# Optimization experiments

Measured on AMD Instinct MI355X. Metric: run time of the kernel, lower is better.

## Reference

```python
import jax, jax.numpy as jnp
import numpy as np

Q_HEADS, KV_HEADS, HEAD_DIM, WINDOW = 16, 4, 128, 512
HIDDEN = 2048
ROPE_BASE = 10000.0


def _rope_tables(T, head_dim, dtype):
    half = head_dim // 2
    inv_freq = 1.0 / (ROPE_BASE ** (jnp.arange(half, dtype=jnp.float32) / half))
    t = jnp.arange(T, dtype=jnp.float32)
    freqs = jnp.outer(t, inv_freq)  # [T, half]
    return jnp.cos(freqs).astype(dtype), jnp.sin(freqs).astype(dtype)


def _apply_rope(x, cos, sin):
    # x: [B, T, H, D]; cos/sin: [T, D//2] -> broadcast [1, T, 1, D//2]
    c = cos[None, :, None, :]
    s = sin[None, :, None, :]
    x1, x2 = jnp.split(x, 2, axis=-1)
    return jnp.concatenate([x1 * c - x2 * s, x1 * s + x2 * c], axis=-1)


def setup_inputs() -> dict:
    key = jax.random.key(0)
    ks = jax.random.split(key, 5)
    B, T = 1, 4096
    x = jax.random.normal(ks[0], (B, T, HIDDEN), dtype=jnp.float32)
    sc = 0.02
    wq = jax.random.normal(ks[1], (Q_HEADS * HEAD_DIM, HIDDEN), dtype=jnp.float32) * sc
    wk = jax.random.normal(ks[2], (KV_HEADS * HEAD_DIM, HIDDEN), dtype=jnp.float32) * sc
    wv = jax.random.normal(ks[3], (KV_HEADS * HEAD_DIM, HIDDEN), dtype=jnp.float32) * sc
    wo = jax.random.normal(ks[4], (HIDDEN, Q_HEADS * HEAD_DIM), dtype=jnp.float32) * sc
    return {"x": x, "wq": wq, "wk": wk, "wv": wv, "wo": wo}


def reference(x, wq, wk, wv, wo):
    B, T, _ = x.shape
    reps = Q_HEADS // KV_HEADS
    scale = 1.0 / np.sqrt(HEAD_DIM)

    q = jnp.einsum('bth,oh->bto', x, wq).reshape(B, T, Q_HEADS, HEAD_DIM)
    k = jnp.einsum('bth,oh->bto', x, wk).reshape(B, T, KV_HEADS, HEAD_DIM)
    v = jnp.einsum('bth,oh->bto', x, wv).reshape(B, T, KV_HEADS, HEAD_DIM)

    cos, sin = _rope_tables(T, HEAD_DIM, x.dtype)
    q = _apply_rope(q, cos, sin)
    k = _apply_rope(k, cos, sin)

    # GQA without materializing repeated K/V: group q as [B,T,KVH,reps,D]
    qg = q.reshape(B, T, KV_HEADS, reps, HEAD_DIM)
    scores = jnp.einsum('btgrd,bsgd->bgrts', qg, k) * scale  # [B,KVH,reps,T,T]

    idx = jnp.arange(T)
    # allowed: causal (s <= t) AND within window (t - s <= WINDOW)
    allowed = (idx[None, :] <= idx[:, None]) & (idx[:, None] - idx[None, :] <= WINDOW)
    scores = jnp.where(allowed[None, None, None], scores, jnp.finfo(scores.dtype).min)
    probs = jax.nn.softmax(scores, axis=-1)

    out = jnp.einsum('bgrts,bsgd->btgrd', probs, v)  # [B,T,KVH,reps,D]
    out = out.reshape(B, T, Q_HEADS * HEAD_DIM)
    return jnp.einsum('bto,ho->bth', out, wo)
```

## Files before the change

### kernel.cpp

```cpp
#include <hip/hip_runtime.h>

typedef __attribute__((ext_vector_type(8))) short short8;
typedef __attribute__((ext_vector_type(4))) float f32x4;
typedef __attribute__((ext_vector_type(4))) unsigned short u16x4;

__device__ __forceinline__ unsigned short f2b(float f) {
  unsigned int u = __float_as_uint(f);
  u += 0x7fffu + ((u >> 16) & 1u);
  return (unsigned short)(u >> 16);
}
__device__ __forceinline__ void glds16(const void* g, void* l) {
  __builtin_amdgcn_global_load_lds(
      (const __attribute__((address_space(1))) unsigned int*)g,
      (__attribute__((address_space(3))) unsigned int*)l, 16, 0, 0);
}

__global__ __launch_bounds__(256) void cast_all(const float* __restrict__ x,
                                                const float* __restrict__ wq,
                                                const float* __restrict__ wk,
                                                const float* __restrict__ wv,
                                                const float* __restrict__ wo,
                                                unsigned short* __restrict__ dst) {
  const int i = blockIdx.x * 256 + threadIdx.x;
  const float* s;
  int off;
  if (i < 2097152)      { s = x;  off = i; }
  else if (i < 3145728) { s = wq; off = i - 2097152; }
  else if (i < 3407872) { s = wk; off = i - 3145728; }
  else if (i < 3670016) { s = wv; off = i - 3407872; }
  else                  { s = wo; off = i - 3670016; }
  f32x4 v = ((const f32x4*)s)[off];
  u16x4 o;
  o[0] = f2b(v[0]); o[1] = f2b(v[1]); o[2] = f2b(v[2]); o[3] = f2b(v[3]);
  ((u16x4*)dst)[i] = o;
}

__global__ __launch_bounds__(512, 2) void gemm256(
    const unsigned short* __restrict__ A, const unsigned short* __restrict__ B,
    const int K, const int mode,
    unsigned short* __restrict__ qb, unsigned short* __restrict__ kb,
    unsigned short* __restrict__ vtg, float* __restrict__ Cout, const int N) {
  extern __shared__ char smem[];
  const int tid = threadIdx.x;
  const int w = tid >> 6, lane = tid & 63;
  const int quad = lane >> 4, l15 = lane & 15;
  const int wm = w >> 2, wn = w & 3;
  const int m0 = blockIdx.x * 256, n0 = blockIdx.y * 256;
  const int nkt = K >> 6;

  int nb[4];
#pragma unroll
  for (int ni = 0; ni < 4; ++ni) {
    const int bbi = (wn & 1) * 4 + ni;
    nb[ni] = mode ? ((bbi & 1) ? 4 + (bbi >> 1) : (bbi >> 1)) : bbi;
  }

  const int fragOff = l15 * 64 + ((quad * 16) ^ ((l15 & 8) << 2));
  char* const aWave = smem + wm * 16384;
  char* const bWave = smem + 32768 + (wn >> 1) * 16384;

  const int sr = lane >> 2;
  const int sc = ((lane & 3) * 8) ^ ((lane & 32) ? 16 : 0);

  auto stageA = [&](int buf, int h, int kt) {
#pragma unroll
    for (int j = 0; j < 2; ++j) {
      const int s = j * 8 + w;
      glds16(A + (size_t)(m0 + h * 128 + (s >> 1) * 16 + sr) * K + kt * 64 + (s & 1) * 32 + sc,
             smem + buf * 65536 + h * 16384 + s * 1024);
    }
  };
  auto stageB = [&](int buf, int h, int kt) {
#pragma unroll
    for (int j = 0; j < 2; ++j) {
      const int s = j * 8 + w;
      glds16(B + (size_t)(n0 + h * 128 + (s >> 1) * 16 + sr) * K + kt * 64 + (s & 1) * 32 + sc,
             smem + buf * 65536 + 32768 + h * 16384 + s * 1024);
    }
  };

  f32x4 acc[8][4];
  const f32x4 fz = {0.f, 0.f, 0.f, 0.f};
#pragma unroll
  for (int i = 0; i < 8; ++i)
#pragma unroll
    for (int j = 0; j < 4; ++j) acc[i][j] = fz;

  stageB(0, 0, 0); stageA(0, 0, 0); stageA(0, 1, 0); stageB(0, 1, 0);
  stageB(1, 0, 1); stageA(1, 0, 1);
  asm volatile("s_waitcnt vmcnt(4)" ::: "memory");
  __builtin_amdgcn_s_barrier();

  short8 af[4][2], blo[2][2], bhi[2][2];

#define MFMA_Q(MOFF, NOFF, BF)                                                   \
  _Pragma("unroll") for (int mi = 0; mi < 4; ++mi)                               \
  _Pragma("unroll") for (int ni = 0; ni < 2; ++ni)                               \
  _Pragma("unroll") for (int kk = 0; kk < 2; ++kk)                               \
      acc[(MOFF) + mi][(NOFF) + ni] = __builtin_amdgcn_mfma_f32_16x16x32_bf16(   \
          af[mi][kk], BF[ni][kk], acc[(MOFF) + mi][(NOFF) + ni], 0, 0, 0);

  for (int T = 0; T < nkt; ++T) {
    const int c = T & 1;
    char* const ab = aWave + c * 65536;
    char* const bp = bWave + c * 65536;

#pragma unroll
    for (int mi = 0; mi < 4; ++mi)
#pragma unroll
      for (int kk = 0; kk < 2; ++kk)
        af[mi][kk] = *(const short8*)(ab + (mi * 2 + kk) * 1024 + fragOff);
#pragma unroll
    for (int ni = 0; ni < 2; ++ni)
#pragma unroll
      for (int kk = 0; kk < 2; ++kk)
        blo[ni][kk] = *(const short8*)(bp + (nb[ni] * 2 + kk) * 1024 + fragOff);
    if (T + 1 < nkt) stageA(c ^ 1, 1, T + 1);
    __builtin_amdgcn_s_barrier();
    asm volatile("s_waitcnt lgkmcnt(0)" ::: "memory");
    __builtin_amdgcn_s_setprio(1);
    MFMA_Q(0, 0, blo)
    __builtin_amdgcn_s_setprio(0);
    __builtin_amdgcn_s_barrier();

#pragma unroll
    for (int ni = 0; ni < 2; ++ni)
#pragma unroll
      for (int kk = 0; kk < 2; ++kk)
        bhi[ni][kk] = *(const short8*)(bp + (nb[ni + 2] * 2 + kk) * 1024 + fragOff);
    if (T + 1 < nkt) stageB(c ^ 1, 1, T + 1);
    __builtin_amdgcn_s_barrier();
    asm volatile("s_waitcnt lgkmcnt(0)" ::: "memory");
    __builtin_amdgcn_s_setprio(1);
    MFMA_Q(0, 2, bhi)
    __builtin_amdgcn_s_setprio(0);
    __builtin_amdgcn_s_barrier();

#pragma unroll
    for (int mi = 0; mi < 4; ++mi)
#pragma unroll
      for (int kk = 0; kk < 2; ++kk)
        af[mi][kk] = *(const short8*)(ab + ((mi + 4) * 2 + kk) * 1024 + fragOff);
    if (T + 2 < nkt) stageB(c, 0, T + 2);
    __builtin_amdgcn_s_barrier();
    asm volatile("s_waitcnt lgkmcnt(0)" ::: "memory");
    __builtin_amdgcn_s_setprio(1);
    MFMA_Q(4, 2, bhi)
    __builtin_amdgcn_s_setprio(0);
    __builtin_amdgcn_s_barrier();

    if (T + 2 < nkt) stageA(c, 0, T + 2);
    __builtin_amdgcn_s_barrier();
    __builtin_amdgcn_s_setprio(1);
    MFMA_Q(4, 0, blo)
    __builtin_amdgcn_s_setprio(0);
    if (T + 2 < nkt) { asm volatile("s_waitcnt vmcnt(4)" ::: "memory"); }
    else             { asm volatile("s_waitcnt vmcnt(0)" ::: "memory"); }
    __builtin_amdgcn_s_barrier();
  }
#undef MFMA_Q

  if (mode == 0) {
    const int colBase = n0 + wn * 64;
#pragma unroll
    for (int mi = 0; mi < 8; ++mi) {
      const int row = m0 + wm * 128 + mi * 16 + quad * 4;
#pragma unroll
      for (int ni = 0; ni < 4; ++ni) {
        const int col = colBase + ni * 16 + l15;
#pragma unroll
        for (int r = 0; r < 4; ++r)
          Cout[(size_t)(row + r) * N + col] = acc[mi][ni][r];
      }
    }
    return;
  }

  const int y = blockIdx.y;
  const int tb0 = m0 + wm * 128;
  if (y >= 10) {
    const int g = (y - 10) * 2 + (wn >> 1);
#pragma unroll
    for (int mi = 0; mi < 8; ++mi) {
      const int tb = tb0 + mi * 16 + quad * 4;
#pragma unroll
      for (int ni = 0; ni < 4; ++ni) {
        const int d = nb[ni] * 16 + l15;
        u16x4 o;
#pragma unroll
        for (int r = 0; r < 4; ++r) o[r] = f2b(acc[mi][ni][r]);
        *(u16x4*)(vtg + (size_t)(g * 128 + d) * 4096 + tb) = o;
      }
    }
  } else {
    unsigned short* dst;
    int stride, hoff;
    if (y < 8) { dst = qb; stride = 2048; hoff = (y * 2 + (wn >> 1)) * 128; }
    else       { dst = kb; stride = 512;  hoff = ((y - 8) * 2 + (wn >> 1)) * 128; }
    const float c2 = 0.20762050593045889f;
    const float inv2pi = 0.15915494309189535f;
#pragma unroll
    for (int j = 0; j < 2; ++j) {
      const int i = ((wn & 1) * 2 + j) * 16 + l15;
      const float inv_rev = exp2f(-(float)i * c2) * inv2pi;
#pragma unroll
      for (int mi = 0; mi < 8; ++mi) {
#pragma unroll
        for (int r = 0; r < 4; ++r) {
          const int t = tb0 + mi * 16 + quad * 4 + r;
          float rev = (float)t * inv_rev;
          rev -= floorf(rev);
          const float sn = __builtin_amdgcn_sinf(rev);
          const float cs = __builtin_amdgcn_cosf(rev);
          const float x1 = acc[mi][2 * j][r], x2 = acc[mi][2 * j + 1][r];
          unsigned short* p = dst + (size_t)t * stride + hoff + i;
          p[0]  = f2b(x1 * cs - x2 * sn);
          p[64] = f2b(x1 * sn + x2 * cs);
        }
      }
    }
  }
}

__global__ __launch_bounds__(512) void attn_fwd(const unsigned short* __restrict__ qp,
                                                const unsigned short* __restrict__ kp,
                                                const unsigned short* __restrict__ vtg,
                                                unsigned short* __restrict__ op) {
  __shared__ unsigned short Ks[2][4][1024];
  __shared__ unsigned short Vt[2][4096];
  const int tid = threadIdx.x;
  const int w = tid >> 6, lane = tid & 63;
  const int quad = lane >> 4, l15 = lane & 15;
  const int t0 = blockIdx.x * 64;
  const int g = blockIdx.y;
  const int h = g * 4 + (w & 3);
  const int t0w = t0 + (w >> 2) * 32;
  const f32x4 fzero = {0.f, 0.f, 0.f, 0.f};
  const float scale = 0.088388347648318447f;
  const float NEG_INF = -__builtin_inff();

  short8 qf[4][2];
#pragma unroll
  for (int qt = 0; qt < 2; qt++) {
    const unsigned short* qrow = qp + (size_t)(t0w + qt * 16 + l15) * 2048 + h * 128 + quad * 8;
#pragma unroll
    for (int kb = 0; kb < 4; kb++) qf[kb][qt] = *(const short8*)(qrow + kb * 32);
  }

  f32x4 oacc[8][2];
#pragma unroll
  for (int db = 0; db < 8; db++) { oacc[db][0] = fzero; oacc[db][1] = fzero; }
  float Mrow[2] = {-1.0e30f, -1.0e30f}, Lrow[2] = {0.f, 0.f};

  const int s_begin = (t0 >= 512) ? (t0 - 512) : 0;
  const int nch = ((t0 + 63 - s_begin) >> 5) + 1;

  const int r4 = lane >> 2, c4 = lane & 3;
#define ATTN_STAGE(s0_, b_)                                                              \
  {                                                                                      \
    const int s0v = (s0_);                                                               \
    if (w < 4) {                                                                         \
      _Pragma("unroll")                                                                  \
      for (int p = 0; p < 2; p++)                                                        \
        glds16(kp + (size_t)(s0v + p * 16 + r4) * 512 + g * 128 + w * 32 + c4 * 8,       \
               &Ks[b_][w][p * 512]);                                                     \
    } else {                                                                             \
      const int wv = w - 4;                                                              \
      _Pragma("unroll")                                                                  \
      for (int p = 0; p < 2; p++)                                                        \
        glds16(vtg + (size_t)(g * 128 + wv * 32 + p * 16 + r4) * 4096 + s0v + c4 * 8,    \
               &Vt[b_][wv * 1024 + p * 512]);                                            \
    }                                                                                    \
  }

  ATTN_STAGE(s_begin, 0);

  for (int c = 0; c < nch; ++c) {
    const int s0 = s_begin + c * 32;
    const int b = c & 1;
    __syncthreads();
    if (c + 1 < nch) ATTN_STAGE(s_begin + (c + 1) * 32, (c + 1) & 1);

    if (s0 + 31 >= t0w - 512 && s0 <= t0w + 31) {
      f32x4 sacc[2][2];
      sacc[0][0] = fzero; sacc[0][1] = fzero; sacc[1][0] = fzero; sacc[1][1] = fzero;
      const int permBase = ((l15 >> 2) << 3) + (l15 & 3);
#pragma unroll
      for (int kb = 0; kb < 4; kb++) {
        short8 af0 = *(const short8*)&Ks[b][kb][(permBase + 0) * 32 + quad * 8];
        short8 af1 = *(const short8*)&Ks[b][kb][(permBase + 4) * 32 + quad * 8];
        sacc[0][0] = __builtin_amdgcn_mfma_f32_16x16x32_bf16(af0, qf[kb][0], sacc[0][0], 0, 0, 0);
        sacc[0][1] = __builtin_amdgcn_mfma_f32_16x16x32_bf16(af0, qf[kb][1], sacc[0][1], 0, 0, 0);
        sacc[1][0] = __builtin_amdgcn_mfma_f32_16x16x32_bf16(af1, qf[kb][0], sacc[1][0], 0, 0, 0);
        sacc[1][1] = __builtin_amdgcn_mfma_f32_16x16x32_bf16(af1, qf[kb][1], sacc[1][1], 0, 0, 0);
      }

      short8 pb[2];
      float alpha[2];
#pragma unroll
      for (int qt = 0; qt < 2; qt++) {
        const int tq = t0w + qt * 16 + l15;
        float vals[8];
        float cmax = NEG_INF;
#pragma unroll
        for (int kt = 0; kt < 2; kt++)
#pragma unroll
          for (int r = 0; r < 4; r++) {
            const int s = s0 + quad * 8 + kt * 4 + r;
            const bool ok = (unsigned)(tq - s) <= 512u;
            const float v = ok ? sacc[kt][qt][r] * scale : NEG_INF;
            vals[kt * 4 + r] = v;
            cmax = fmaxf(cmax, v);
          }
        cmax = fmaxf(cmax, __shfl_xor(cmax, 16));
        cmax = fmaxf(cmax, __shfl_xor(cmax, 32));
        const float Mnew = fmaxf(Mrow[qt], cmax);
        alpha[qt] = __expf(Mrow[qt] - Mnew);
        Mrow[qt] = Mnew;
        float csum = 0.f;
#pragma unroll
        for (int j = 0; j < 8; j++) {
          const float p = __expf(vals[j] - Mnew);
          csum += p;
          pb[qt][j] = (short)f2b(p);
        }
        csum += __shfl_xor(csum, 16);
        csum += __shfl_xor(csum, 32);
        Lrow[qt] = Lrow[qt] * alpha[qt] + csum;
      }

#pragma unroll
      for (int db = 0; db < 8; db++) {
        short8 vf = *(const short8*)&Vt[b][(db * 16 + l15) * 32 + quad * 8];
#pragma unroll
        for (int qt = 0; qt < 2; qt++) {
          oacc[db][qt][0] *= alpha[qt]; oacc[db][qt][1] *= alpha[qt];
          oacc[db][qt][2] *= alpha[qt]; oacc[db][qt][3] *= alpha[qt];
          oacc[db][qt] = __builtin_amdgcn_mfma_f32_16x16x32_bf16(vf, pb[qt], oacc[db][qt], 0, 0, 0);
        }
      }
    }
  }
#undef ATTN_STAGE

#pragma unroll
  for (int qt = 0; qt < 2; qt++) {
    const float invL = 1.f / Lrow[qt];
    unsigned short* orow = op + (size_t)(t0w + qt * 16 + l15) * 2048 + h * 128;
#pragma unroll
    for (int db = 0; db < 8; db++) {
      u16x4 o;
#pragma unroll
      for (int r = 0; r < 4; r++) o[r] = f2b(oacc[db][qt][r] * invL);
      *(u16x4*)(orow + db * 16 + quad * 4) = o;
    }
  }
}

extern "C" void kernel_launch(void* const* d_in, const int* in_sizes, int n_in,
                              void* d_out, int out_size, void* d_ws, size_t ws_size,
                              hipStream_t stream) {
  const float* x  = (const float*)d_in[0];
  const float* wq = (const float*)d_in[1];
  const float* wk = (const float*)d_in[2];
  const float* wv = (const float*)d_in[3];
  const float* wo = (const float*)d_in[4];
  float* out = (float*)d_out;
  char* ws = (char*)d_ws;

  unsigned short* xb    = (unsigned short*)(ws + 0);
  unsigned short* wqkv  = (unsigned short*)(ws + 16777216);
  unsigned short* wob   = (unsigned short*)(ws + 29360128);
  unsigned short* qb    = (unsigned short*)(ws + 37748736);
  unsigned short* kbuf  = (unsigned short*)(ws + 54525952);
  unsigned short* vtg   = (unsigned short*)(ws + 58720256);
  unsigned short* attnb = xb;

  static bool attr_done = false;
  if (!attr_done) {
    hipFuncSetAttribute(reinterpret_cast<const void*>(gemm256),
                        hipFuncAttributeMaxDynamicSharedMemorySize, 131072);
    attr_done = true;
  }

  cast_all<<<18432, 256, 0, stream>>>(x, wq, wk, wv, wo, (unsigned short*)ws);

  gemm256<<<dim3(16, 12), 512, 131072, stream>>>(xb, wqkv, 2048, 1,
                                                 qb, kbuf, vtg, nullptr, 0);

  attn_fwd<<<dim3(64, 4), 512, 0, stream>>>(qb, kbuf, vtg, attnb);

  gemm256<<<dim3(16, 8), 512, 131072, stream>>>(attnb, wob, 2048, 0,
                                                nullptr, nullptr, nullptr, out, 2048);
}
```

Before: 274.3 us.

## Rework GEMM main loop into unrolled two-stage pipeline with constant K

Rewrites the GEMM K-loop to hard-code K=N=2048, unroll by two iterations with compile-time buffer indices, and change the order of LDS fragment reads, global-to-LDS staging and MFMA quarters. Fragment reads for the next quarter are issued right after the current MFMA block, so LDS latency overlaps compute. Staging always runs, with the tile index clamped to avoid branches at the loop tail. This removes per-iteration address arithmetic and branches, but redundant tail loads and the hard-coded dimensions make the kernel valid only for this shape.

Result: faster. 261.8 us (-4.5%).

```diff
diff --git a/kernel.cpp b/kernel.cpp
--- a/kernel.cpp
+++ b/kernel.cpp
@@ -37,16 +37,15 @@
 
 __global__ __launch_bounds__(512, 2) void gemm256(
     const unsigned short* __restrict__ A, const unsigned short* __restrict__ B,
-    const int K, const int mode,
+    const int Karg, const int mode,
     unsigned short* __restrict__ qb, unsigned short* __restrict__ kb,
-    unsigned short* __restrict__ vtg, float* __restrict__ Cout, const int N) {
+    unsigned short* __restrict__ vtg, float* __restrict__ Cout, const int Narg) {
   extern __shared__ char smem[];
   const int tid = threadIdx.x;
   const int w = tid >> 6, lane = tid & 63;
   const int quad = lane >> 4, l15 = lane & 15;
   const int wm = w >> 2, wn = w & 3;
   const int m0 = blockIdx.x * 256, n0 = blockIdx.y * 256;
-  const int nkt = K >> 6;
 
   int nb[4];
 #pragma unroll
@@ -61,23 +60,35 @@
 
   const int sr = lane >> 2;
   const int sc = ((lane & 3) * 8) ^ ((lane & 32) ? 16 : 0);
-
-  auto stageA = [&](int buf, int h, int kt) {
-#pragma unroll
-    for (int j = 0; j < 2; ++j) {
-      const int s = j * 8 + w;
-      glds16(A + (size_t)(m0 + h * 128 + (s >> 1) * 16 + sr) * K + kt * 64 + (s & 1) * 32 + sc,
-             smem + buf * 65536 + h * 16384 + s * 1024);
-    }
-  };
-  auto stageB = [&](int buf, int h, int kt) {
-#pragma unroll
-    for (int j = 0; j < 2; ++j) {
-      const int s = j * 8 + w;
-      glds16(B + (size_t)(n0 + h * 128 + (s >> 1) * 16 + sr) * K + kt * 64 + (s & 1) * 32 + sc,
-             smem + buf * 65536 + 32768 + h * 16384 + s * 1024);
-    }
-  };
+  const unsigned short* const Abase = A + (size_t)(m0 + (w >> 1) * 16 + sr) * 2048 + (w & 1) * 32 + sc;
+  const unsigned short* const Bbase = B + (size_t)(n0 + (w >> 1) * 16 + sr) * 2048 + (w & 1) * 32 + sc;
+
+#define BARF()                            \
+  asm volatile("" ::: "memory");          \
+  __builtin_amdgcn_s_barrier();           \
+  asm volatile("" ::: "memory");
+
+#define STAGE_AJ(h, tt, jj)                                                              \
+  {                                                                                      \
+    const int t_ = ((tt) < 32) ? (tt) : 31;                                              \
+    glds16(Abase + (size_t)(h) * (128 * 2048) + (jj) * (64 * 2048) + (size_t)t_ * 64,    \
+           smem + (t_ & 1) * 65536 + (h) * 16384 + (jj) * 8192 + w * 1024);              \
+  }
+#define STAGE_B2(h, tt)                                                                  \
+  {                                                                                      \
+    const int t_ = ((tt) < 32) ? (tt) : 31;                                              \
+    char* const d_ = smem + (t_ & 1) * 65536 + 32768 + (h) * 16384 + w * 1024;           \
+    glds16(Bbase + (size_t)(h) * (128 * 2048) + (size_t)t_ * 64, d_);                    \
+    glds16(Bbase + (size_t)(h) * (128 * 2048) + (64 * 2048) + (size_t)t_ * 64, d_ + 8192); \
+  }
+#define RD_A(dst, c, MI0)                                                                \
+  _Pragma("unroll") for (int mi = 0; mi < 4; ++mi)                                       \
+  _Pragma("unroll") for (int kk = 0; kk < 2; ++kk)                                       \
+      dst[mi][kk] = *(const short8*)(aWave + (c) * 65536 + (((MI0) + mi) * 2 + kk) * 1024 + fragOff);
+#define RD_B(dst, c, NI0)                                                                \
+  _Pragma("unroll") for (int ni = 0; ni < 2; ++ni)                                       \
+  _Pragma("unroll") for (int kk = 0; kk < 2; ++kk)                                       \
+      dst[ni][kk] = *(const short8*)(bWave + (c) * 65536 + (nb[(NI0) + ni] * 2 + kk) * 1024 + fragOff);
 
   f32x4 acc[8][4];
   const f32x4 fz = {0.f, 0.f, 0.f, 0.f};
@@ -85,11 +96,6 @@
   for (int i = 0; i < 8; ++i)
 #pragma unroll
     for (int j = 0; j < 4; ++j) acc[i][j] = fz;
-
-  stageB(0, 0, 0); stageA(0, 0, 0); stageA(0, 1, 0); stageB(0, 1, 0);
-  stageB(1, 0, 1); stageA(1, 0, 1);
-  asm volatile("s_waitcnt vmcnt(4)" ::: "memory");
-  __builtin_amdgcn_s_barrier();
 
   short8 af[4][2], blo[2][2], bhi[2][2];
 
@@ -100,65 +106,49 @@
       acc[(MOFF) + mi][(NOFF) + ni] = __builtin_amdgcn_mfma_f32_16x16x32_bf16(   \
           af[mi][kk], BF[ni][kk], acc[(MOFF) + mi][(NOFF) + ni], 0, 0, 0);
 
-  for (int T = 0; T < nkt; ++T) {
-    const int c = T & 1;
-    char* const ab = aWave + c * 65536;
-    char* const bp = bWave + c * 65536;
-
-#pragma unroll
-    for (int mi = 0; mi < 4; ++mi)
-#pragma unroll
-      for (int kk = 0; kk < 2; ++kk)
-        af[mi][kk] = *(const short8*)(ab + (mi * 2 + kk) * 1024 + fragOff);
-#pragma unroll
-    for (int ni = 0; ni < 2; ++ni)
-#pragma unroll
-      for (int kk = 0; kk < 2; ++kk)
-        blo[ni][kk] = *(const short8*)(bp + (nb[ni] * 2 + kk) * 1024 + fragOff);
-    if (T + 1 < nkt) stageA(c ^ 1, 1, T + 1);
-    __builtin_amdgcn_s_barrier();
-    asm volatile("s_waitcnt lgkmcnt(0)" ::: "memory");
-    __builtin_amdgcn_s_setprio(1);
-    MFMA_Q(0, 0, blo)
-    __builtin_amdgcn_s_setprio(0);
-    __builtin_amdgcn_s_barrier();
-
-#pragma unroll
-    for (int ni = 0; ni < 2; ++ni)
-#pragma unroll
-      for (int kk = 0; kk < 2; ++kk)
-        bhi[ni][kk] = *(const short8*)(bp + (nb[ni + 2] * 2 + kk) * 1024 + fragOff);
-    if (T + 1 < nkt) stageB(c ^ 1, 1, T + 1);
-    __builtin_amdgcn_s_barrier();
-    asm volatile("s_waitcnt lgkmcnt(0)" ::: "memory");
-    __builtin_amdgcn_s_setprio(1);
-    MFMA_Q(0, 2, bhi)
-    __builtin_amdgcn_s_setprio(0);
-    __builtin_amdgcn_s_barrier();
-
-#pragma unroll
-    for (int mi = 0; mi < 4; ++mi)
-#pragma unroll
-      for (int kk = 0; kk < 2; ++kk)
-        af[mi][kk] = *(const short8*)(ab + ((mi + 4) * 2 + kk) * 1024 + fragOff);
-    if (T + 2 < nkt) stageB(c, 0, T + 2);
-    __builtin_amdgcn_s_barrier();
-    asm volatile("s_waitcnt lgkmcnt(0)" ::: "memory");
-    __builtin_amdgcn_s_setprio(1);
-    MFMA_Q(4, 2, bhi)
-    __builtin_amdgcn_s_setprio(0);
-    __builtin_amdgcn_s_barrier();
-
-    if (T + 2 < nkt) stageA(c, 0, T + 2);
-    __builtin_amdgcn_s_barrier();
-    __builtin_amdgcn_s_setprio(1);
-    MFMA_Q(4, 0, blo)
-    __builtin_amdgcn_s_setprio(0);
-    if (T + 2 < nkt) { asm volatile("s_waitcnt vmcnt(4)" ::: "memory"); }
-    else             { asm volatile("s_waitcnt vmcnt(0)" ::: "memory"); }
-    __builtin_amdgcn_s_barrier();
-  }
+  STAGE_AJ(0, 0, 0) STAGE_AJ(1, 0, 0) STAGE_B2(0, 0) STAGE_B2(1, 0) STAGE_AJ(0, 0, 1) STAGE_AJ(1, 0, 1)
+  STAGE_AJ(0, 1, 0) STAGE_AJ(1, 1, 0) STAGE_B2(0, 1) STAGE_B2(1, 1) STAGE_AJ(0, 1, 1) STAGE_AJ(1, 1, 1)
+  asm volatile("s_waitcnt vmcnt(8)" ::: "memory");
+  __builtin_amdgcn_s_barrier();
+  asm volatile("" ::: "memory");
+  RD_A(af, 0, 0)
+  RD_B(blo, 0, 0)
+
+#define HALF(c, tt)                                                                  \
+                                                                             \
+  BARF()                                                                             \
+  __builtin_amdgcn_s_setprio(1); MFMA_Q(0, 0, blo) __builtin_amdgcn_s_setprio(0);    \
+  RD_B(bhi, (c), 2)                                                                  \
+  BARF()                                                                             \
+   STAGE_AJ(0, (tt) + 2, 0) STAGE_AJ(1, (tt) + 2, 0)                         \
+  BARF()                                                                             \
+  __builtin_amdgcn_s_setprio(1); MFMA_Q(0, 2, bhi) __builtin_amdgcn_s_setprio(0);    \
+  RD_A(af, (c), 4)                                                                   \
+  BARF()                                                                             \
+   STAGE_B2(0, (tt) + 2) STAGE_B2(1, (tt) + 2)                               \
+  BARF()                                                                             \
+  __builtin_amdgcn_s_setprio(1); MFMA_Q(4, 2, bhi) __builtin_amdgcn_s_setprio(0);    \
+  BARF()                                                                             \
+   STAGE_AJ(0, (tt) + 2, 1) STAGE_AJ(1, (tt) + 2, 1)                         \
+  BARF()                                                                             \
+  __builtin_amdgcn_s_setprio(1); MFMA_Q(4, 0, blo) __builtin_amdgcn_s_setprio(0);    \
+  asm volatile("s_waitcnt vmcnt(8)" ::: "memory");                                   \
+  RD_A(af, (c) ^ 1, 0)                                                               \
+  RD_B(blo, (c) ^ 1, 0)
+
+#pragma unroll 1
+  for (int T = 0; T < 32; T += 2) {
+    HALF(0, T)
+    HALF(1, T + 1)
+  }
+  asm volatile("s_waitcnt vmcnt(0)" ::: "memory");
+#undef HALF
 #undef MFMA_Q
+#undef RD_A
+#undef RD_B
+#undef STAGE_AJ
+#undef STAGE_B2
+#undef BARF
 
   if (mode == 0) {
     const int colBase = n0 + wn * 64;
@@ -170,7 +160,7 @@
         const int col = colBase + ni * 16 + l15;
 #pragma unroll
         for (int r = 0; r < 4; ++r)
-          Cout[(size_t)(row + r) * N + col] = acc[mi][ni][r];
+          Cout[(size_t)(row + r) * 2048 + col] = acc[mi][ni][r];
       }
     }
     return;
```
